# Performance work log

Hardware: AMD Instinct MI355X
Metric: run time of the kernel (lower is better)

## Reference

```python
import jax, jax.numpy as jnp
import numpy as np

N1 = 8192; N2 = 8192; E = 131072
D_IN = 128; H = 256; T = 32; B = 16
GCN_DIMS = [(D_IN, H), (H, H), (H, H)]


def _gcn_conv(x, edge_index, W):
    # PyG GCNConv (bias=False): add self-loops, symmetric D^-1/2 (A+I) D^-1/2 normalization.
    n = x.shape[0]
    h = x @ W
    loop = jnp.arange(n, dtype=edge_index.dtype)
    src = jnp.concatenate([edge_index[0], loop])
    dst = jnp.concatenate([edge_index[1], loop])
    deg = jax.ops.segment_sum(jnp.ones(dst.shape[0], h.dtype), dst, num_segments=n)
    dinv = jnp.where(deg > 0, jax.lax.rsqrt(deg), 0.0)
    norm = dinv[src] * dinv[dst]
    return jax.ops.segment_sum(norm[:, None] * h[src], dst, num_segments=n)


def _layer(f1, f2, ei1, ei2, Wg, Wu, bu, last):
    c1 = _gcn_conv(f1, ei1, Wg)
    c2 = _gcn_conv(f2, ei2, Wg)
    sim = f1 @ f2.T                      # [N1, N2] 'dot' similarity
    a1 = jax.nn.softmax(sim, axis=1)     # row softmax
    a2 = jax.nn.softmax(sim, axis=0)     # col softmax
    att1 = a1 @ f2                       # [N1, d]
    att2 = a2.T @ f1                     # [N2, d]
    g1 = jnp.concatenate([c1, f1, f1 - att1], axis=1) @ Wu + bu
    g2 = jnp.concatenate([c2, f2, f2 - att2], axis=1) @ Wu + bu
    if last:
        return g1, g2                    # last layer: no tanh, no dropout
    return jnp.tanh(g1), jnp.tanh(g2)    # dropout is a no-op in eval mode


def _forward(f1, f2, ei1, ei2, avg_v, gcn_Ws, upd_Ws, upd_bs,
             gated_W, gated_b, tn_W, tn_Wb, tn_b, fc1_W, fc1_b, sc_W, sc_b):
    n_layers = len(gcn_Ws)
    for i in range(n_layers):
        f1, f2 = _layer(f1, f2, ei1, ei2, gcn_Ws[i], upd_Ws[i], upd_bs[i],
                        last=(i == n_layers - 1))
    # gated readout: sum(sigmoid(gated(x)) * x)
    p1 = jnp.sum(jax.nn.sigmoid(f1 @ gated_W + gated_b) * f1, axis=0)  # [H]
    p2 = jnp.sum(jax.nn.sigmoid(f2 @ gated_W + gated_b) * f2, axis=0)  # [H]
    # NTN (TensorNetworkModule)
    scoring = jnp.einsum('i,ijt,j->t', p1, tn_W, p2)                   # bilinear term [T]
    block = tn_Wb @ jnp.concatenate([p1, p2])                          # [T]
    ntn = jax.nn.relu(scoring + block + tn_b)
    s = jnp.tanh(ntn @ fc1_W + fc1_b)                                  # [B]
    score = jax.nn.sigmoid(s @ sc_W + sc_b)                            # [1]
    pre_ged = -jnp.log(score) * avg_v                                  # target_mode='exp'
    return score.reshape(-1), pre_ged.reshape(-1)


def setup_inputs():
    key = jax.random.key(0)
    ks = jax.random.split(key, 32)
    rn = lambda k, sh, s=0.05: jax.random.normal(k, sh, dtype=jnp.float32) * s
    inp = {
        'features_1': jax.random.normal(ks[0], (N1, D_IN), dtype=jnp.float32),
        'features_2': jax.random.normal(ks[1], (N2, D_IN), dtype=jnp.float32),
        'edge_index_1': jax.random.randint(ks[2], (2, E), 0, N1, dtype=jnp.int32),
        'edge_index_2': jax.random.randint(ks[3], (2, E), 0, N2, dtype=jnp.int32),
        'avg_v': jnp.full((1,), 12.0, dtype=jnp.float32),
    }
    for i, (di, do) in enumerate(GCN_DIMS):
        inp[f'gcn_W{i}'] = rn(ks[4 + i], (di, do))
        inp[f'upd_W{i}'] = rn(ks[8 + i], (2 * di + do, do))
        inp[f'upd_b{i}'] = jnp.zeros((do,), jnp.float32)
    inp['gated_W'] = rn(ks[12], (H, H)); inp['gated_b'] = jnp.zeros((H,), jnp.float32)
    inp['tn_W'] = rn(ks[13], (H, H, T))
    inp['tn_Wb'] = rn(ks[14], (T, 2 * H)); inp['tn_b'] = jnp.zeros((T,), jnp.float32)
    inp['fc1_W'] = rn(ks[15], (T, B)); inp['fc1_b'] = jnp.zeros((B,), jnp.float32)
    inp['sc_W'] = rn(ks[16], (B, 1)); inp['sc_b'] = jnp.zeros((1,), jnp.float32)
    return inp


def reference(features_1, features_2, edge_index_1, edge_index_2, avg_v,
              gcn_W0, gcn_W1, gcn_W2, upd_W0, upd_W1, upd_W2,
              upd_b0, upd_b1, upd_b2, gated_W, gated_b,
              tn_W, tn_Wb, tn_b, fc1_W, fc1_b, sc_W, sc_b):
    return _forward(features_1, features_2, edge_index_1, edge_index_2, avg_v,
                    [gcn_W0, gcn_W1, gcn_W2], [upd_W0, upd_W1, upd_W2],
                    [upd_b0, upd_b1, upd_b2], gated_W, gated_b,
                    tn_W, tn_Wb, tn_b, fc1_W, fc1_b, sc_W, sc_b)
```

## Files before the change

kernel.cpp:

```cpp
#include <hip/hip_runtime.h>
#include <hip/hip_bf16.h>
#include <stdint.h>

#define NN 8192
#define EDG 131072
#define NSPLIT 4

typedef __attribute__((ext_vector_type(8))) short bf16x8;
typedef __attribute__((ext_vector_type(4))) float f32x4;
typedef unsigned short us;

__device__ __forceinline__ us f2bf(float f) {
  union { float f; unsigned u; } v; v.f = f;
  return (us)((v.u + 0x7fffu + ((v.u >> 16) & 1u)) >> 16);
}

__device__ __forceinline__ us f2bf_trunc(float f) {
  union { float f; unsigned u; } v; v.f = f;
  return (us)(v.u >> 16);
}

__device__ __forceinline__ float bf2f(us u) {
  union { unsigned u; float f; } v; v.u = ((unsigned)u) << 16;
  return v.f;
}

__device__ __forceinline__ void load_lds16(const void* g, void* l) {
  __builtin_amdgcn_global_load_lds(
      (__attribute__((address_space(1))) void*)(uintptr_t)g,
      (__attribute__((address_space(3))) void*)(uintptr_t)l,
      16, 0, 0);
}

template <int EPI>
__global__ __launch_bounds__(256) void gemm_k(
    const us* __restrict__ A, int lda, const us* __restrict__ Bt, int ldb,
    const float* __restrict__ bias, void* __restrict__ Cv, int ldc, int K) {
  __shared__ alignas(16) us As[64 * 32];
  __shared__ alignas(16) us Bs[128 * 32];
  const int t = threadIdx.x;
  const int wave = t >> 6, lane = t & 63;
  const int wrow = wave * 16;
  const int lrow = lane & 15, quad = lane >> 4;
  const int rowBase = blockIdx.x * 64;
  const int colBase = blockIdx.y * 128;
  const int sr = t >> 2, sch = t & 3;

  f32x4 acc[8];
#pragma unroll
  for (int j = 0; j < 8; j++) acc[j] = f32x4{0.f, 0.f, 0.f, 0.f};

  for (int kb = 0; kb < K; kb += 32) {
    __syncthreads();
    const us* asrc = A + (size_t)(rowBase + sr) * lda + kb + sch * 8;
    load_lds16(asrc, (char*)As + t * 16);
    const us* bsrc = Bt + (size_t)(colBase + sr) * ldb + kb + sch * 8;
    load_lds16(bsrc, (char*)Bs + t * 16);
    load_lds16(bsrc + (size_t)64 * ldb, (char*)Bs + t * 16 + 4096);
    __syncthreads();
    bf16x8 af = *(const bf16x8*)&As[(wrow + lrow) * 32 + quad * 8];
#pragma unroll
    for (int j = 0; j < 8; j++) {
      bf16x8 bfr = *(const bf16x8*)&Bs[(j * 16 + lrow) * 32 + quad * 8];
      acc[j] = __builtin_amdgcn_mfma_f32_16x16x32_bf16(af, bfr, acc[j], 0, 0, 0);
    }
  }

#pragma unroll
  for (int j = 0; j < 8; j++) {
    int col = colBase + j * 16 + lrow;
#pragma unroll
    for (int r = 0; r < 4; r++) {
      int row = rowBase + wrow + quad * 4 + r;
      size_t idx = (size_t)row * ldc + col;
      float v = acc[j][r];
      if (EPI == 0) ((float*)Cv)[idx] = v;
      else if (EPI == 2) ((float*)Cv)[idx] = v + bias[col];
      else if (EPI == 4) ((us*)Cv)[idx] = f2bf(v + bias[col]);
      else ((us*)Cv)[idx] = f2bf(tanhf(v + bias[col]));
    }
  }
}

template <int DIN>
__global__ __launch_bounds__(256, (DIN == 128) ? 3 : 2) void flash_att(
    const us* __restrict__ Q, const us* __restrict__ K,
    const us* __restrict__ Vt, us* __restrict__ Opart,
    float* __restrict__ mpart, float* __restrict__ lpart, int kvPerSplit) {
  constexpr int NKC = DIN / 32;
  constexpr int OJ = DIN / 16;
  __shared__ alignas(16) us As[2][64 * 32];
  __shared__ alignas(16) us KB[2][128 * 32];
  __shared__ alignas(16) us Vs[2][DIN * 32];
  us* Ps = &KB[0][0];

  const int t = threadIdx.x;
  const int wave = t >> 6, lane = t & 63;
  const int wrow = wave * 16;
  const int lrow = lane & 15, quad = lane >> 4;
  const int rowBase = blockIdx.x * 64;
  const int split = blockIdx.y;
  const int kv0 = split * kvPerSplit;
  const int sr = t >> 2, sch = t & 3;
  const int pkey = ((lrow >> 2) ^ lrow) & 3;

  auto stageQ = [&](int kc, int buf) {
    const us* qsrc = Q + (size_t)(rowBase + sr) * DIN + kc * 32 + sch * 8;
    load_lds16(qsrc, (char*)&As[buf][0] + t * 16);
  };
  auto stageK = [&](int kt, int kc, int buf) {
    const us* ksrc = K + (size_t)(kt + sr) * DIN + kc * 32 + sch * 8;
    load_lds16(ksrc, (char*)&KB[buf][0] + t * 16);
    load_lds16(ksrc + (size_t)64 * DIN, (char*)&KB[buf][0] + t * 16 + 4096);
  };
  auto stageV = [&](int kt, int cc, int buf) {
#pragma unroll
    for (int p = 0; p < DIN / 64; p++) {
      const us* vsrc = Vt + (size_t)(p * 64 + sr) * NN + kt + cc * 32 + sch * 8;
      load_lds16(vsrc, (char*)&Vs[buf][0] + p * 4096 + t * 16);
    }
  };

  stageQ(0, 0);
  stageV(kv0, 0, 0);

  float m_i[4], l_i[4];
#pragma unroll
  for (int r = 0; r < 4; r++) { m_i[r] = -3.0e38f; l_i[r] = 0.f; }
  f32x4 accO[OJ];
#pragma unroll
  for (int j = 0; j < OJ; j++) accO[j] = f32x4{0.f, 0.f, 0.f, 0.f};

  for (int kt = kv0; kt < kv0 + kvPerSplit; kt += 128) {
    __syncthreads();
    stageK(kt, 0, 0);

    f32x4 accS[8];
#pragma unroll
    for (int j = 0; j < 8; j++) accS[j] = f32x4{0.f, 0.f, 0.f, 0.f};
    for (int kc = 0; kc < NKC; kc++) {
      const int buf = kc & 1;
      __syncthreads();
      if (kc + 1 < NKC) { stageK(kt, kc + 1, buf ^ 1); stageQ(kc + 1, buf ^ 1); }
      bf16x8 af = *(const bf16x8*)&As[buf][(wrow + lrow) * 32 + quad * 8];
#pragma unroll
      for (int j = 0; j < 8; j++) {
        bf16x8 bfr = *(const bf16x8*)&KB[buf][(j * 16 + lrow) * 32 + quad * 8];
        accS[j] = __builtin_amdgcn_mfma_f32_16x16x32_bf16(af, bfr, accS[j], 0, 0, 0);
      }
    }

    float alpha[4];
#pragma unroll
    for (int r = 0; r < 4; r++) {
      float v = accS[0][r];
#pragma unroll
      for (int j = 1; j < 8; j++) v = fmaxf(v, accS[j][r]);
#pragma unroll
      for (int mask = 1; mask < 16; mask <<= 1) v = fmaxf(v, __shfl_xor(v, mask));
      float mn = fmaxf(m_i[r], v);
      alpha[r] = __expf(m_i[r] - mn);
      m_i[r] = mn;
    }
    __syncthreads();
    float ts[4] = {0.f, 0.f, 0.f, 0.f};
#pragma unroll
    for (int j = 0; j < 8; j++)
#pragma unroll
      for (int r = 0; r < 4; r++) {
        float p = __expf(accS[j][r] - m_i[r]);
        ts[r] += p;
        int prow = wrow + quad * 4 + r;
        int key = (quad ^ r) & 3;
        int g = (j * 16 + lrow) >> 3;
        Ps[prow * 128 + ((g ^ (key << 1)) << 3) + (lrow & 7)] = f2bf_trunc(p);
      }
#pragma unroll
    for (int r = 0; r < 4; r++) {
      float v = ts[r];
#pragma unroll
      for (int mask = 1; mask < 16; mask <<= 1) v += __shfl_xor(v, mask);
      l_i[r] = l_i[r] * alpha[r] + v;
    }
#pragma unroll
    for (int j = 0; j < OJ; j++)
#pragma unroll
      for (int r = 0; r < 4; r++) accO[j][r] *= alpha[r];

    const bool hasNext = (kt + 128 < kv0 + kvPerSplit);
    for (int cc = 0; cc < 4; cc++) {
      if (cc) __syncthreads();
      if (cc + 1 < 4) stageV(kt, cc + 1, (cc + 1) & 1);
      else if (hasNext) { stageV(kt + 128, 0, 0); stageQ(0, 0); }
      const int gk = cc * 4 + quad;
      bf16x8 af = *(const bf16x8*)&Ps[(wrow + lrow) * 128 + ((gk ^ (pkey << 1)) << 3)];
      const us* vb = &Vs[cc & 1][0];
#pragma unroll
      for (int j = 0; j < OJ; j++) {
        bf16x8 bfr = *(const bf16x8*)&vb[(j * 16 + lrow) * 32 + quad * 8];
        accO[j] = __builtin_amdgcn_mfma_f32_16x16x32_bf16(af, bfr, accO[j], 0, 0, 0);
      }
    }
  }

#pragma unroll
  for (int j = 0; j < OJ; j++)
#pragma unroll
    for (int r = 0; r < 4; r++) {
      int row = rowBase + wrow + quad * 4 + r;
      int col = j * 16 + lrow;
      Opart[((size_t)split * NN + row) * DIN + col] = f2bf(accO[j][r]);
    }
  if (lrow == 0) {
#pragma unroll
    for (int r = 0; r < 4; r++) {
      int row = rowBase + wrow + quad * 4 + r;
      mpart[(size_t)split * NN + row] = m_i[r];
      lpart[(size_t)split * NN + row] = l_i[r];
    }
  }
}

__global__ void merge_cat(const us* __restrict__ Op, const float* __restrict__ mp,
                          const float* __restrict__ lp, const float* __restrict__ cbuf,
                          const us* __restrict__ fbf, us* __restrict__ cat,
                          int din, int W) {
  int i = blockIdx.y;
  int c = blockIdx.x * 256 + threadIdx.x;
  us o;
  if (c < 256) {
    o = f2bf(cbuf[(size_t)i * 256 + c]);
  } else if (c < 256 + din) {
    o = fbf[(size_t)i * din + (c - 256)];
  } else {
    int f = c - 256 - din;
    float m[NSPLIT], w[NSPLIT];
    float M = -3.0e38f;
#pragma unroll
    for (int s = 0; s < NSPLIT; s++) { m[s] = mp[(size_t)s * NN + i]; M = fmaxf(M, m[s]); }
    float L = 0.f;
#pragma unroll
    for (int s = 0; s < NSPLIT; s++) { w[s] = __expf(m[s] - M); L += lp[(size_t)s * NN + i] * w[s]; }
    float a = 0.f;
#pragma unroll
    for (int s = 0; s < NSPLIT; s++)
      a += w[s] * bf2f(Op[((size_t)s * NN + i) * din + f]);
    o = f2bf(bf2f(fbf[(size_t)i * din + f]) - a / L);
  }
  cat[(size_t)i * W + c] = o;
}


__global__ void ws_sentinel(float* out) { out[0] = 12345.0f; out[1] = 12345.0f; }

__global__ void cvt_bf16(const float* __restrict__ in, us* __restrict__ out, int n) {
  int i = (blockIdx.x * 256 + threadIdx.x) * 4;
  if (i < n) {
    f32x4 v = *(const f32x4*)(in + i);
    uint2 p;
    p.x = f2bf(v.x) | ((unsigned)f2bf(v.y) << 16);
    p.y = f2bf(v.z) | ((unsigned)f2bf(v.w) << 16);
    *(uint2*)(out + i) = p;
  }
}

__global__ void transpose_bf16(const float* __restrict__ src, us* __restrict__ dst,
                               int R, int C) {
  __shared__ float tile[32][33];
  int c0 = blockIdx.x * 32, r0 = blockIdx.y * 32;
  int x = threadIdx.x, y = threadIdx.y;
  for (int i = y; i < 32; i += 8) tile[i][x] = src[(size_t)(r0 + i) * C + c0 + x];
  __syncthreads();
  for (int i = y; i < 32; i += 8) dst[(size_t)(c0 + i) * R + r0 + x] = f2bf(tile[x][i]);
}

__global__ void transpose_bb(const us* __restrict__ src, us* __restrict__ dst,
                             int R, int C) {
  __shared__ us tile[32][33];
  int c0 = blockIdx.x * 32, r0 = blockIdx.y * 32;
  int x = threadIdx.x, y = threadIdx.y;
  for (int i = y; i < 32; i += 8) tile[i][x] = src[(size_t)(r0 + i) * C + c0 + x];
  __syncthreads();
  for (int i = y; i < 32; i += 8) dst[(size_t)(c0 + i) * R + r0 + x] = tile[x][i];
}

__global__ void deg_count(const int* __restrict__ dst, int* __restrict__ deg) {
  int e = blockIdx.x * 256 + threadIdx.x;
  atomicAdd(&deg[dst[e]], 1);
}

__global__ void make_dinv(const int* __restrict__ deg, float* __restrict__ dinv) {
  int v = blockIdx.x * 256 + threadIdx.x;
  dinv[v] = rsqrtf((float)(deg[v] + 1));
}

__global__ void scan_deg(const int* __restrict__ deg, int* __restrict__ rowstart) {
  __shared__ int part[1024];
  int t = threadIdx.x;
  int base = t * 8;
  int local[8];
  int s = 0;
#pragma unroll
  for (int i = 0; i < 8; i++) { local[i] = s; s += deg[base + i]; }
  part[t] = s;
  __syncthreads();
  for (int off = 1; off < 1024; off <<= 1) {
    int v = (t >= off) ? part[t - off] : 0;
    __syncthreads();
    part[t] += v;
    __syncthreads();
  }
  int offset = (t == 0) ? 0 : part[t - 1];
#pragma unroll
  for (int i = 0; i < 8; i++) rowstart[base + i] = offset + local[i];
  if (t == 1023) rowstart[8192] = offset + s;
}

__global__ void csr_fill(const int* __restrict__ src, const int* __restrict__ dst,
                         int* __restrict__ cursor, int* __restrict__ csr_src) {
  int e = blockIdx.x * 256 + threadIdx.x;
  int pos = atomicAdd(&cursor[dst[e]], 1);
  csr_src[pos] = src[e];
}

__global__ __launch_bounds__(256) void gcn_agg(
    const int* __restrict__ rowstart, const int* __restrict__ csr_src,
    const float* __restrict__ dinv, const float* __restrict__ h,
    float* __restrict__ c) {
  int node = blockIdx.x * 4 + (threadIdx.x >> 6);
  int lane = threadIdx.x & 63;
  float dn = dinv[node];
  f32x4 acc = *(const f32x4*)(h + (size_t)node * 256 + lane * 4);
  float w0 = dn * dn;
  acc.x *= w0; acc.y *= w0; acc.z *= w0; acc.w *= w0;
  int s0 = rowstart[node], s1 = rowstart[node + 1];
  for (int j = s0; j < s1; j++) {
    int s = csr_src[j];
    float w = dinv[s] * dn;
    f32x4 v = *(const f32x4*)(h + (size_t)s * 256 + lane * 4);
    acc.x += w * v.x; acc.y += w * v.y; acc.z += w * v.z; acc.w += w * v.w;
  }
  *(f32x4*)(c + (size_t)node * 256 + lane * 4) = acc;
}

__global__ void gated_pool(const float* __restrict__ q, const us* __restrict__ f,
                           float* __restrict__ p) {
  int col = threadIdx.x;
  int r0 = blockIdx.x * 128;
  float a = 0.f;
  for (int i = r0; i < r0 + 128; i++) {
    float qv = q[(size_t)i * 256 + col];
    a += bf2f(f[(size_t)i * 256 + col]) / (1.f + __expf(-qv));
  }
  atomicAdd(&p[col], a);
}

__global__ void ntn_bilinear(const float* __restrict__ p1, const float* __restrict__ tnW,
                             float* __restrict__ tmp) {
  int c = blockIdx.x * 256 + threadIdx.x;
  float a = 0.f;
#pragma unroll 8
  for (int i = 0; i < 256; i++) a += p1[i] * tnW[(size_t)i * 8192 + c];
  tmp[c] = a;
}

__global__ void ntn_final(const float* __restrict__ tmp, const float* __restrict__ p1,
                          const float* __restrict__ p2, const float* __restrict__ tnWb,
                          const float* __restrict__ tnb, const float* __restrict__ fc1W,
                          const float* __restrict__ fc1b, const float* __restrict__ scW,
                          const float* __restrict__ scb, const float* __restrict__ avgv,
                          float* __restrict__ out) {
  __shared__ float pc[512];
  __shared__ float ntn[32];
  __shared__ float sarr[16];
  int t = threadIdx.x;
  pc[t] = p1[t];
  pc[256 + t] = p2[t];
  __syncthreads();
  if (t < 32) {
    float sc = 0.f;
    for (int j = 0; j < 256; j++) sc += tmp[j * 32 + t] * pc[256 + j];
    float bl = 0.f;
    for (int k = 0; k < 512; k++) bl += tnWb[t * 512 + k] * pc[k];
    float v = sc + bl + tnb[t];
    ntn[t] = v > 0.f ? v : 0.f;
  }
  __syncthreads();
  if (t < 16) {
    float a = fc1b[t];
    for (int i = 0; i < 32; i++) a += ntn[i] * fc1W[i * 16 + t];
    sarr[t] = tanhf(a);
  }
  __syncthreads();
  if (t == 0) {
    float a = scb[0];
    for (int b = 0; b < 16; b++) a += sarr[b] * scW[b];
    float score = 1.f / (1.f + expf(-a));
    out[0] = score;
    out[1] = -logf(score) * avgv[0];
  }
}


extern "C" void kernel_launch(void* const* d_in, const int* in_sizes, int n_in,
                              void* d_out, int out_size, void* d_ws, size_t ws_size,
                              hipStream_t stream) {
  (void)in_sizes; (void)n_in; (void)out_size;
  const float* feat1 = (const float*)d_in[0];
  const float* feat2 = (const float*)d_in[1];
  const int* ei1 = (const int*)d_in[2];
  const int* ei2 = (const int*)d_in[3];
  const float* avgv = (const float*)d_in[4];
  const float* gcnW[3] = {(const float*)d_in[5], (const float*)d_in[8], (const float*)d_in[11]};
  const float* updW[3] = {(const float*)d_in[6], (const float*)d_in[9], (const float*)d_in[12]};
  const float* updb[3] = {(const float*)d_in[7], (const float*)d_in[10], (const float*)d_in[13]};
  const float* gatedW = (const float*)d_in[14];
  const float* gatedb = (const float*)d_in[15];
  const float* tnW = (const float*)d_in[16];
  const float* tnWb = (const float*)d_in[17];
  const float* tnb = (const float*)d_in[18];
  const float* fc1W = (const float*)d_in[19];
  const float* fc1b = (const float*)d_in[20];
  const float* scW = (const float*)d_in[21];
  const float* scb = (const float*)d_in[22];
  float* out = (float*)d_out;

  char* wp = (char*)d_ws;
  auto take = [&](size_t b) { char* p = wp; wp += (b + 255) & ~(size_t)255; return p; };
  us* Op = (us*)take((size_t)NSPLIT * NN * 256 * 2);
  us* cat1 = (us*)take((size_t)NN * 768 * 2);
  us* cat2 = (us*)take((size_t)NN * 768 * 2);
  us* fA1 = (us*)take((size_t)NN * 256 * 2);
  us* fA2 = (us*)take((size_t)NN * 256 * 2);
  us* fB1 = (us*)take((size_t)NN * 256 * 2);
  us* fB2 = (us*)take((size_t)NN * 256 * 2);
  us* f1bT = (us*)take((size_t)NN * 256 * 2);
  us* f2bT = (us*)take((size_t)NN * 256 * 2);
  float* h1 = (float*)take((size_t)NN * 256 * 4);
  float* h2 = (float*)take((size_t)NN * 256 * 4);
  float* c1 = (float*)take((size_t)NN * 256 * 4);
  float* c2 = (float*)take((size_t)NN * 256 * 4);
  us* WgT[3], *WuT[3];
  for (int l = 0; l < 3; l++) WgT[l] = (us*)take(256 * 256 * 2);
  for (int l = 0; l < 3; l++) WuT[l] = (us*)take(256 * 768 * 2);
  us* gWT = (us*)take(256 * 256 * 2);
  int* deg1 = (int*)take(NN * 4);
  int* deg2 = (int*)take(NN * 4);
  float* dinv1 = (float*)take(NN * 4);
  float* dinv2 = (float*)take(NN * 4);
  int* rs1 = (int*)take((NN + 1) * 4);
  int* rs2 = (int*)take((NN + 1) * 4);
  int* cur1 = (int*)take(NN * 4);
  int* cur2 = (int*)take(NN * 4);
  int* csr1 = (int*)take((size_t)EDG * 4);
  int* csr2 = (int*)take((size_t)EDG * 4);
  float* mp = (float*)take((size_t)NSPLIT * NN * 4);
  float* lp = (float*)take((size_t)NSPLIT * NN * 4);
  float* p1 = (float*)take(1024);
  float* p2 = (float*)take(1024);
  float* tmp = (float*)take(NN * 4);

  size_t need = (size_t)(wp - (char*)d_ws);
  if (need > ws_size) {
    ws_sentinel<<<1, 1, 0, stream>>>(out);
    return;
  }

  hipMemsetAsync(deg1, 0, NN * 4, stream);
  hipMemsetAsync(deg2, 0, NN * 4, stream);
  deg_count<<<EDG / 256, 256, 0, stream>>>(ei1 + EDG, deg1);
  deg_count<<<EDG / 256, 256, 0, stream>>>(ei2 + EDG, deg2);
  make_dinv<<<NN / 256, 256, 0, stream>>>(deg1, dinv1);
  make_dinv<<<NN / 256, 256, 0, stream>>>(deg2, dinv2);
  scan_deg<<<1, 1024, 0, stream>>>(deg1, rs1);
  scan_deg<<<1, 1024, 0, stream>>>(deg2, rs2);
  hipMemcpyAsync(cur1, rs1, NN * 4, hipMemcpyDeviceToDevice, stream);
  hipMemcpyAsync(cur2, rs2, NN * 4, hipMemcpyDeviceToDevice, stream);
  csr_fill<<<EDG / 256, 256, 0, stream>>>(ei1, ei1 + EDG, cur1, csr1);
  csr_fill<<<EDG / 256, 256, 0, stream>>>(ei2, ei2 + EDG, cur2, csr2);

  for (int l = 0; l < 3; l++) {
    int din = (l == 0) ? 128 : 256;
    int W = 256 + 2 * din;
    transpose_bf16<<<dim3(8, din / 32), dim3(32, 8), 0, stream>>>(gcnW[l], WgT[l], din, 256);
    transpose_bf16<<<dim3(8, W / 32), dim3(32, 8), 0, stream>>>(updW[l], WuT[l], W, 256);
  }
  transpose_bf16<<<dim3(8, 8), dim3(32, 8), 0, stream>>>(gatedW, gWT, 256, 256);

  us* f1 = fA1; us* f2 = fA2;
  us* fn1 = fB1; us* fn2 = fB2;
  cvt_bf16<<<NN * 128 / 1024, 256, 0, stream>>>(feat1, f1, NN * 128);
  cvt_bf16<<<NN * 128 / 1024, 256, 0, stream>>>(feat2, f2, NN * 128);

  for (int l = 0; l < 3; l++) {
    const int din = (l == 0) ? 128 : 256;
    const int W = 256 + 2 * din;

    if (l == 0) {
      transpose_bf16<<<dim3(din / 32, NN / 32), dim3(32, 8), 0, stream>>>(feat1, f1bT, NN, din);
      transpose_bf16<<<dim3(din / 32, NN / 32), dim3(32, 8), 0, stream>>>(feat2, f2bT, NN, din);
    } else {
      transpose_bb<<<dim3(din / 32, NN / 32), dim3(32, 8), 0, stream>>>(f1, f1bT, NN, din);
      transpose_bb<<<dim3(din / 32, NN / 32), dim3(32, 8), 0, stream>>>(f2, f2bT, NN, din);
    }

    gemm_k<0><<<dim3(128, 2), 256, 0, stream>>>(f1, din, WgT[l], din, nullptr, h1, 256, din);
    gemm_k<0><<<dim3(128, 2), 256, 0, stream>>>(f2, din, WgT[l], din, nullptr, h2, 256, din);

    gcn_agg<<<NN / 4, 256, 0, stream>>>(rs1, csr1, dinv1, h1, c1);
    gcn_agg<<<NN / 4, 256, 0, stream>>>(rs2, csr2, dinv2, h2, c2);

    if (l == 0) {
      flash_att<128><<<dim3(NN / 64, NSPLIT), 256, 0, stream>>>(f1, f2, f2bT, Op, mp, lp, NN / NSPLIT);
      merge_cat<<<dim3(W / 256, NN), 256, 0, stream>>>(Op, mp, lp, c1, f1, cat1, din, W);
      flash_att<128><<<dim3(NN / 64, NSPLIT), 256, 0, stream>>>(f2, f1, f1bT, Op, mp, lp, NN / NSPLIT);
      merge_cat<<<dim3(W / 256, NN), 256, 0, stream>>>(Op, mp, lp, c2, f2, cat2, din, W);
    } else {
      flash_att<256><<<dim3(NN / 64, NSPLIT), 256, 0, stream>>>(f1, f2, f2bT, Op, mp, lp, NN / NSPLIT);
      merge_cat<<<dim3(W / 256, NN), 256, 0, stream>>>(Op, mp, lp, c1, f1, cat1, din, W);
      flash_att<256><<<dim3(NN / 64, NSPLIT), 256, 0, stream>>>(f2, f1, f1bT, Op, mp, lp, NN / NSPLIT);
      merge_cat<<<dim3(W / 256, NN), 256, 0, stream>>>(Op, mp, lp, c2, f2, cat2, din, W);
    }

    if (l < 2) {
      gemm_k<5><<<dim3(128, 2), 256, 0, stream>>>(cat1, W, WuT[l], W, updb[l], fn1, 256, W);
      gemm_k<5><<<dim3(128, 2), 256, 0, stream>>>(cat2, W, WuT[l], W, updb[l], fn2, 256, W);
    } else {
      gemm_k<4><<<dim3(128, 2), 256, 0, stream>>>(cat1, W, WuT[l], W, updb[l], fn1, 256, W);
      gemm_k<4><<<dim3(128, 2), 256, 0, stream>>>(cat2, W, WuT[l], W, updb[l], fn2, 256, W);
    }
    us* s;
    s = f1; f1 = fn1; fn1 = s;
    s = f2; f2 = fn2; fn2 = s;
  }

  gemm_k<2><<<dim3(128, 2), 256, 0, stream>>>(f1, 256, gWT, 256, gatedb, c1, 256, 256);
  gemm_k<2><<<dim3(128, 2), 256, 0, stream>>>(f2, 256, gWT, 256, gatedb, c2, 256, 256);
  hipMemsetAsync(p1, 0, 256 * 4, stream);
  hipMemsetAsync(p2, 0, 256 * 4, stream);
  gated_pool<<<64, 256, 0, stream>>>(c1, f1, p1);
  gated_pool<<<64, 256, 0, stream>>>(c2, f2, p2);

  ntn_bilinear<<<32, 256, 0, stream>>>(p1, tnW, tmp);
  ntn_final<<<1, 256, 0, stream>>>(tmp, p1, p2, tnWb, tnb, fc1W, fc1b, scW, scb, avgv, out);
}
```

Measured before the change: 1.209 ms.

## Batch both graphs into single launches and store GCN intermediates in bf16

Each pair of per-graph kernels (gemm, transpose, gcn aggregation, flash attention, merge, pooling, CSR build) becomes one launch, with a grid dimension selecting graph 1 or 2. This removes launch overhead and doubles the grid size, which helps fill the GPU on small kernels. The GCN path now keeps h and the aggregated output in bf16 and folds the source-side dinv scaling into the gemm epilogue. That halves gather traffic but adds bf16 rounding on the intermediates. The attention Op/m/l buffers are doubled so both directions can run concurrently.

```diff
diff --git a/kernel.cpp b/kernel.cpp
--- a/kernel.cpp
+++ b/kernel.cpp
@@ -33,11 +33,16 @@
 }
 
 template <int EPI>
-__global__ __launch_bounds__(256) void gemm_k(
-    const us* __restrict__ A, int lda, const us* __restrict__ Bt, int ldb,
-    const float* __restrict__ bias, void* __restrict__ Cv, int ldc, int K) {
+__global__ __launch_bounds__(256) void gemm2(
+    const us* __restrict__ A1, const us* __restrict__ A2, int lda,
+    const us* __restrict__ Bt, int ldb,
+    const float* __restrict__ b1, const float* __restrict__ b2,
+    void* __restrict__ C1, void* __restrict__ C2, int ldc, int K) {
   __shared__ alignas(16) us As[64 * 32];
   __shared__ alignas(16) us Bs[128 * 32];
+  const us* A = blockIdx.z ? A2 : A1;
+  const float* bias = blockIdx.z ? b2 : b1;
+  void* Cv = blockIdx.z ? C2 : C1;
   const int t = threadIdx.x;
   const int wave = t >> 6, lane = t & 63;
   const int wrow = wave * 16;
@@ -77,22 +82,32 @@
       if (EPI == 0) ((float*)Cv)[idx] = v;
       else if (EPI == 2) ((float*)Cv)[idx] = v + bias[col];
       else if (EPI == 4) ((us*)Cv)[idx] = f2bf(v + bias[col]);
-      else ((us*)Cv)[idx] = f2bf(tanhf(v + bias[col]));
+      else if (EPI == 5) ((us*)Cv)[idx] = f2bf(tanhf(v + bias[col]));
+      else ((us*)Cv)[idx] = f2bf(v * bias[row]);
     }
   }
 }
 
 template <int DIN>
 __global__ __launch_bounds__(256, (DIN == 128) ? 3 : 2) void flash_att(
-    const us* __restrict__ Q, const us* __restrict__ K,
-    const us* __restrict__ Vt, us* __restrict__ Opart,
-    float* __restrict__ mpart, float* __restrict__ lpart, int kvPerSplit) {
+    const us* __restrict__ f1, const us* __restrict__ f2,
+    const us* __restrict__ f1T, const us* __restrict__ f2T,
+    us* __restrict__ Op, float* __restrict__ mp, float* __restrict__ lp,
+    int kvPerSplit) {
   constexpr int NKC = DIN / 32;
   constexpr int OJ = DIN / 16;
   __shared__ alignas(16) us As[2][64 * 32];
   __shared__ alignas(16) us KB[2][128 * 32];
   __shared__ alignas(16) us Vs[2][DIN * 32];
   us* Ps = &KB[0][0];
+
+  const int dir = blockIdx.z;
+  const us* Q = dir ? f2 : f1;
+  const us* K = dir ? f1 : f2;
+  const us* Vt = dir ? f1T : f2T;
+  us* Opart = Op + (size_t)dir * NSPLIT * NN * DIN;
+  float* mpart = mp + (size_t)dir * NSPLIT * NN;
+  float* lpart = lp + (size_t)dir * NSPLIT * NN;
 
   const int t = threadIdx.x;
   const int wave = t >> 6, lane = t & 63;
@@ -172,7 +187,7 @@
         ts[r] += p;
         int prow = wrow + quad * 4 + r;
         int key = (quad ^ r) & 3;
-        int g = (j * 16 + lrow) >> 3;
+        int g = 2 * j + (lrow >> 3);
         Ps[prow * 128 + ((g ^ (key << 1)) << 3) + (lrow & 7)] = f2bf_trunc(p);
       }
 #pragma unroll
@@ -222,14 +237,23 @@
 }
 
 __global__ void merge_cat(const us* __restrict__ Op, const float* __restrict__ mp,
-                          const float* __restrict__ lp, const float* __restrict__ cbuf,
-                          const us* __restrict__ fbf, us* __restrict__ cat,
+                          const float* __restrict__ lp,
+                          const us* __restrict__ cb1, const us* __restrict__ cb2,
+                          const us* __restrict__ f1, const us* __restrict__ f2,
+                          us* __restrict__ cat1, us* __restrict__ cat2,
                           int din, int W) {
+  const int z = blockIdx.z;
+  const us* Ops = Op + (size_t)z * NSPLIT * NN * din;
+  const float* mm = mp + (size_t)z * NSPLIT * NN;
+  const float* ll = lp + (size_t)z * NSPLIT * NN;
+  const us* cbuf = z ? cb2 : cb1;
+  const us* fbf = z ? f2 : f1;
+  us* cat = z ? cat2 : cat1;
   int i = blockIdx.y;
   int c = blockIdx.x * 256 + threadIdx.x;
   us o;
   if (c < 256) {
-    o = f2bf(cbuf[(size_t)i * 256 + c]);
+    o = cbuf[(size_t)i * 256 + c];
   } else if (c < 256 + din) {
     o = fbf[(size_t)i * din + (c - 256)];
   } else {
@@ -237,14 +261,14 @@
     float m[NSPLIT], w[NSPLIT];
     float M = -3.0e38f;
 #pragma unroll
-    for (int s = 0; s < NSPLIT; s++) { m[s] = mp[(size_t)s * NN + i]; M = fmaxf(M, m[s]); }
+    for (int s = 0; s < NSPLIT; s++) { m[s] = mm[(size_t)s * NN + i]; M = fmaxf(M, m[s]); }
     float L = 0.f;
 #pragma unroll
-    for (int s = 0; s < NSPLIT; s++) { w[s] = __expf(m[s] - M); L += lp[(size_t)s * NN + i] * w[s]; }
+    for (int s = 0; s < NSPLIT; s++) { w[s] = __expf(m[s] - M); L += ll[(size_t)s * NN + i] * w[s]; }
     float a = 0.f;
 #pragma unroll
     for (int s = 0; s < NSPLIT; s++)
-      a += w[s] * bf2f(Op[((size_t)s * NN + i) * din + f]);
+      a += w[s] * bf2f(Ops[((size_t)s * NN + i) * din + f]);
     o = f2bf(bf2f(fbf[(size_t)i * din + f]) - a / L);
   }
   cat[(size_t)i * W + c] = o;
@@ -253,7 +277,10 @@
 
 __global__ void ws_sentinel(float* out) { out[0] = 12345.0f; out[1] = 12345.0f; }
 
-__global__ void cvt_bf16(const float* __restrict__ in, us* __restrict__ out, int n) {
+__global__ void cvt2(const float* __restrict__ i1, const float* __restrict__ i2,
+                     us* __restrict__ o1, us* __restrict__ o2, int n) {
+  const float* in = blockIdx.y ? i2 : i1;
+  us* out = blockIdx.y ? o2 : o1;
   int i = (blockIdx.x * 256 + threadIdx.x) * 4;
   if (i < n) {
     f32x4 v = *(const f32x4*)(in + i);
@@ -274,27 +301,50 @@
   for (int i = y; i < 32; i += 8) dst[(size_t)(c0 + i) * R + r0 + x] = f2bf(tile[x][i]);
 }
 
-__global__ void transpose_bb(const us* __restrict__ src, us* __restrict__ dst,
-                             int R, int C) {
-  __shared__ us tile[32][33];
+__global__ void transpose_bf2(const float* __restrict__ s1, const float* __restrict__ s2,
+                              us* __restrict__ d1, us* __restrict__ d2, int R, int C) {
+  __shared__ float tile[32][33];
+  const float* src = blockIdx.z ? s2 : s1;
+  us* dst = blockIdx.z ? d2 : d1;
   int c0 = blockIdx.x * 32, r0 = blockIdx.y * 32;
   int x = threadIdx.x, y = threadIdx.y;
   for (int i = y; i < 32; i += 8) tile[i][x] = src[(size_t)(r0 + i) * C + c0 + x];
   __syncthreads();
+  for (int i = y; i < 32; i += 8) dst[(size_t)(c0 + i) * R + r0 + x] = f2bf(tile[x][i]);
+}
+
+__global__ void transpose_bb2(const us* __restrict__ s1, const us* __restrict__ s2,
+                              us* __restrict__ d1, us* __restrict__ d2, int R, int C) {
+  __shared__ us tile[32][33];
+  const us* src = blockIdx.z ? s2 : s1;
+  us* dst = blockIdx.z ? d2 : d1;
+  int c0 = blockIdx.x * 32, r0 = blockIdx.y * 32;
+  int x = threadIdx.x, y = threadIdx.y;
+  for (int i = y; i < 32; i += 8) tile[i][x] = src[(size_t)(r0 + i) * C + c0 + x];
+  __syncthreads();
   for (int i = y; i < 32; i += 8) dst[(size_t)(c0 + i) * R + r0 + x] = tile[x][i];
 }
 
-__global__ void deg_count(const int* __restrict__ dst, int* __restrict__ deg) {
+__global__ void deg_count2(const int* __restrict__ d1, const int* __restrict__ d2,
+                           int* __restrict__ g1, int* __restrict__ g2) {
+  const int* dst = blockIdx.y ? d2 : d1;
+  int* deg = blockIdx.y ? g2 : g1;
   int e = blockIdx.x * 256 + threadIdx.x;
   atomicAdd(&deg[dst[e]], 1);
 }
 
-__global__ void make_dinv(const int* __restrict__ deg, float* __restrict__ dinv) {
+__global__ void make_dinv2(const int* __restrict__ g1, const int* __restrict__ g2,
+                           float* __restrict__ o1, float* __restrict__ o2) {
+  const int* deg = blockIdx.y ? g2 : g1;
+  float* dinv = blockIdx.y ? o2 : o1;
   int v = blockIdx.x * 256 + threadIdx.x;
   dinv[v] = rsqrtf((float)(deg[v] + 1));
 }
 
-__global__ void scan_deg(const int* __restrict__ deg, int* __restrict__ rowstart) {
+__global__ void scan_deg2(const int* __restrict__ g1, const int* __restrict__ g2,
+                          int* __restrict__ r1, int* __restrict__ r2) {
+  const int* deg = blockIdx.x ? g2 : g1;
+  int* rowstart = blockIdx.x ? r2 : r1;
   __shared__ int part[1024];
   int t = threadIdx.x;
   int base = t * 8;
@@ -316,35 +366,54 @@
   if (t == 1023) rowstart[8192] = offset + s;
 }
 
-__global__ void csr_fill(const int* __restrict__ src, const int* __restrict__ dst,
-                         int* __restrict__ cursor, int* __restrict__ csr_src) {
+__global__ void csr_fill2(const int* __restrict__ e1, const int* __restrict__ e2,
+                          int* __restrict__ cu1, int* __restrict__ cu2,
+                          int* __restrict__ c1, int* __restrict__ c2) {
+  const int* ei = blockIdx.y ? e2 : e1;
+  int* cursor = blockIdx.y ? cu2 : cu1;
+  int* csr_src = blockIdx.y ? c2 : c1;
   int e = blockIdx.x * 256 + threadIdx.x;
-  int pos = atomicAdd(&cursor[dst[e]], 1);
-  csr_src[pos] = src[e];
-}
-
-__global__ __launch_bounds__(256) void gcn_agg(
-    const int* __restrict__ rowstart, const int* __restrict__ csr_src,
-    const float* __restrict__ dinv, const float* __restrict__ h,
-    float* __restrict__ c) {
+  int pos = atomicAdd(&cursor[ei[EDG + e]], 1);
+  csr_src[pos] = ei[e];
+}
+
+__global__ __launch_bounds__(256) void gcn_agg2(
+    const int* __restrict__ r1, const int* __restrict__ r2,
+    const int* __restrict__ cs1, const int* __restrict__ cs2,
+    const float* __restrict__ d1, const float* __restrict__ d2,
+    const us* __restrict__ h1, const us* __restrict__ h2,
+    us* __restrict__ o1, us* __restrict__ o2) {
+  const int* rowstart = blockIdx.y ? r2 : r1;
+  const int* csr_src = blockIdx.y ? cs2 : cs1;
+  const float* dinv = blockIdx.y ? d2 : d1;
+  const us* hs = blockIdx.y ? h2 : h1;
+  us* c = blockIdx.y ? o2 : o1;
   int node = blockIdx.x * 4 + (threadIdx.x >> 6);
   int lane = threadIdx.x & 63;
-  float dn = dinv[node];
-  f32x4 acc = *(const f32x4*)(h + (size_t)node * 256 + lane * 4);
-  float w0 = dn * dn;
-  acc.x *= w0; acc.y *= w0; acc.z *= w0; acc.w *= w0;
+  const us* hp = hs + lane * 4;
+  uint2 u = *(const uint2*)(hp + (size_t)node * 256);
+  float a0 = bf2f(u.x & 0xffffu), a1 = bf2f(u.x >> 16);
+  float a2 = bf2f(u.y & 0xffffu), a3 = bf2f(u.y >> 16);
   int s0 = rowstart[node], s1 = rowstart[node + 1];
   for (int j = s0; j < s1; j++) {
     int s = csr_src[j];
-    float w = dinv[s] * dn;
-    f32x4 v = *(const f32x4*)(h + (size_t)s * 256 + lane * 4);
-    acc.x += w * v.x; acc.y += w * v.y; acc.z += w * v.z; acc.w += w * v.w;
-  }
-  *(f32x4*)(c + (size_t)node * 256 + lane * 4) = acc;
-}
-
-__global__ void gated_pool(const float* __restrict__ q, const us* __restrict__ f,
-                           float* __restrict__ p) {
+    uint2 v = *(const uint2*)(hp + (size_t)s * 256);
+    a0 += bf2f(v.x & 0xffffu); a1 += bf2f(v.x >> 16);
+    a2 += bf2f(v.y & 0xffffu); a3 += bf2f(v.y >> 16);
+  }
+  float dn = dinv[node];
+  uint2 o;
+  o.x = f2bf(a0 * dn) | ((unsigned)f2bf(a1 * dn) << 16);
+  o.y = f2bf(a2 * dn) | ((unsigned)f2bf(a3 * dn) << 16);
+  *(uint2*)(c + (size_t)node * 256 + lane * 4) = o;
+}
+
+__global__ void gated_pool2(const float* __restrict__ q1, const float* __restrict__ q2,
+                            const us* __restrict__ f1, const us* __restrict__ f2,
+                            float* __restrict__ o1, float* __restrict__ o2) {
+  const float* q = blockIdx.y ? q2 : q1;
+  const us* f = blockIdx.y ? f2 : f1;
+  float* p = blockIdx.y ? o2 : o1;
   int col = threadIdx.x;
   int r0 = blockIdx.x * 128;
   float a = 0.f;
@@ -427,19 +496,21 @@
 
   char* wp = (char*)d_ws;
   auto take = [&](size_t b) { char* p = wp; wp += (b + 255) & ~(size_t)255; return p; };
-  us* Op = (us*)take((size_t)NSPLIT * NN * 256 * 2);
+  us* Op = (us*)take((size_t)2 * NSPLIT * NN * 256 * 2);
   us* cat1 = (us*)take((size_t)NN * 768 * 2);
   us* cat2 = (us*)take((size_t)NN * 768 * 2);
+  float* q1 = (float*)cat1;
+  float* q2 = (float*)cat2;
   us* fA1 = (us*)take((size_t)NN * 256 * 2);
   us* fA2 = (us*)take((size_t)NN * 256 * 2);
   us* fB1 = (us*)take((size_t)NN * 256 * 2);
   us* fB2 = (us*)take((size_t)NN * 256 * 2);
   us* f1bT = (us*)take((size_t)NN * 256 * 2);
   us* f2bT = (us*)take((size_t)NN * 256 * 2);
-  float* h1 = (float*)take((size_t)NN * 256 * 4);
-  float* h2 = (float*)take((size_t)NN * 256 * 4);
-  float* c1 = (float*)take((size_t)NN * 256 * 4);
-  float* c2 = (float*)take((size_t)NN * 256 * 4);
+  us* hs1 = (us*)take((size_t)NN * 256 * 2);
+  us* hs2 = (us*)take((size_t)NN * 256 * 2);
+  us* cb1 = (us*)take((size_t)NN * 256 * 2);
+  us* cb2 = (us*)take((size_t)NN * 256 * 2);
   us* WgT[3], *WuT[3];
   for (int l = 0; l < 3; l++) WgT[l] = (us*)take(256 * 256 * 2);
   for (int l = 0; l < 3; l++) WuT[l] = (us*)take(256 * 768 * 2);
@@ -454,8 +525,8 @@
   int* cur2 = (int*)take(NN * 4);
   int* csr1 = (int*)take((size_t)EDG * 4);
   int* csr2 = (int*)take((size_t)EDG * 4);
-  float* mp = (float*)take((size_t)NSPLIT * NN * 4);
-  float* lp = (float*)take((size_t)NSPLIT * NN * 4);
+  float* mp = (float*)take((size_t)2 * NSPLIT * NN * 4);
+  float* lp = (float*)take((size_t)2 * NSPLIT * NN * 4);
   float* p1 = (float*)take(1024);
   float* p2 = (float*)take(1024);
   float* tmp = (float*)take(NN * 4);
@@ -468,16 +539,12 @@
 
   hipMemsetAsync(deg1, 0, NN * 4, stream);
   hipMemsetAsync(deg2, 0, NN * 4, stream);
-  deg_count<<<EDG / 256, 256, 0, stream>>>(ei1 + EDG, deg1);
-  deg_count<<<EDG / 256, 256, 0, stream>>>(ei2 + EDG, deg2);
-  make_dinv<<<NN / 256, 256, 0, stream>>>(deg1, dinv1);
-  make_dinv<<<NN / 256, 256, 0, stream>>>(deg2, dinv2);
-  scan_deg<<<1, 1024, 0, stream>>>(deg1, rs1);
-  scan_deg<<<1, 1024, 0, stream>>>(deg2, rs2);
+  deg_count2<<<dim3(EDG / 256, 2), 256, 0, stream>>>(ei1 + EDG, ei2 + EDG, deg1, deg2);
+  make_dinv2<<<dim3(NN / 256, 2), 256, 0, stream>>>(deg1, deg2, dinv1, dinv2);
+  scan_deg2<<<2, 1024, 0, stream>>>(deg1, deg2, rs1, rs2);
   hipMemcpyAsync(cur1, rs1, NN * 4, hipMemcpyDeviceToDevice, stream);
   hipMemcpyAsync(cur2, rs2, NN * 4, hipMemcpyDeviceToDevice, stream);
-  csr_fill<<<EDG / 256, 256, 0, stream>>>(ei1, ei1 + EDG, cur1, csr1);
-  csr_fill<<<EDG / 256, 256, 0, stream>>>(ei2, ei2 + EDG, cur2, csr2);
+  csr_fill2<<<dim3(EDG / 256, 2), 256, 0, stream>>>(ei1, ei2, cur1, cur2, csr1, csr2);
 
   for (int l = 0; l < 3; l++) {
     int din = (l == 0) ? 128 : 256;
@@ -489,57 +556,40 @@
 
   us* f1 = fA1; us* f2 = fA2;
   us* fn1 = fB1; us* fn2 = fB2;
-  cvt_bf16<<<NN * 128 / 1024, 256, 0, stream>>>(feat1, f1, NN * 128);
-  cvt_bf16<<<NN * 128 / 1024, 256, 0, stream>>>(feat2, f2, NN * 128);
+  cvt2<<<dim3(NN * 128 / 1024, 2), 256, 0, stream>>>(feat1, feat2, f1, f2, NN * 128);
 
   for (int l = 0; l < 3; l++) {
     const int din = (l == 0) ? 128 : 256;
     const int W = 256 + 2 * din;
 
-    if (l == 0) {
-      transpose_bf16<<<dim3(din / 32, NN / 32), dim3(32, 8), 0, stream>>>(feat1, f1bT, NN, din);
-      transpose_bf16<<<dim3(din / 32, NN / 32), dim3(32, 8), 0, stream>>>(feat2, f2bT, NN, din);
-    } else {
-      transpose_bb<<<dim3(din / 32, NN / 32), dim3(32, 8), 0, stream>>>(f1, f1bT, NN, din);
-      transpose_bb<<<dim3(din / 32, NN / 32), dim3(32, 8), 0, stream>>>(f2, f2bT, NN, din);
-    }
-
-    gemm_k<0><<<dim3(128, 2), 256, 0, stream>>>(f1, din, WgT[l], din, nullptr, h1, 256, din);
-    gemm_k<0><<<dim3(128, 2), 256, 0, stream>>>(f2, din, WgT[l], din, nullptr, h2, 256, din);
-
-    gcn_agg<<<NN / 4, 256, 0, stream>>>(rs1, csr1, dinv1, h1, c1);
-    gcn_agg<<<NN / 4, 256, 0, stream>>>(rs2, csr2, dinv2, h2, c2);
-
-    if (l == 0) {
-      flash_att<128><<<dim3(NN / 64, NSPLIT), 256, 0, stream>>>(f1, f2, f2bT, Op, mp, lp, NN / NSPLIT);
-      merge_cat<<<dim3(W / 256, NN), 256, 0, stream>>>(Op, mp, lp, c1, f1, cat1, din, W);
-      flash_att<128><<<dim3(NN / 64, NSPLIT), 256, 0, stream>>>(f2, f1, f1bT, Op, mp, lp, NN / NSPLIT);
-      merge_cat<<<dim3(W / 256, NN), 256, 0, stream>>>(Op, mp, lp, c2, f2, cat2, din, W);
-    } else {
-      flash_att<256><<<dim3(NN / 64, NSPLIT), 256, 0, stream>>>(f1, f2, f2bT, Op, mp, lp, NN / NSPLIT);
-      merge_cat<<<dim3(W / 256, NN), 256, 0, stream>>>(Op, mp, lp, c1, f1, cat1, din, W);
-      flash_att<256><<<dim3(NN / 64, NSPLIT), 256, 0, stream>>>(f2, f1, f1bT, Op, mp, lp, NN / NSPLIT);
-      merge_cat<<<dim3(W / 256, NN), 256, 0, stream>>>(Op, mp, lp, c2, f2, cat2, din, W);
-    }
-
-    if (l < 2) {
-      gemm_k<5><<<dim3(128, 2), 256, 0, stream>>>(cat1, W, WuT[l], W, updb[l], fn1, 256, W);
-      gemm_k<5><<<dim3(128, 2), 256, 0, stream>>>(cat2, W, WuT[l], W, updb[l], fn2, 256, W);
-    } else {
-      gemm_k<4><<<dim3(128, 2), 256, 0, stream>>>(cat1, W, WuT[l], W, updb[l], fn1, 256, W);
-      gemm_k<4><<<dim3(128, 2), 256, 0, stream>>>(cat2, W, WuT[l], W, updb[l], fn2, 256, W);
-    }
+    if (l == 0)
+      transpose_bf2<<<dim3(din / 32, NN / 32, 2), dim3(32, 8), 0, stream>>>(feat1, feat2, f1bT, f2bT, NN, din);
+    else
+      transpose_bb2<<<dim3(din / 32, NN / 32, 2), dim3(32, 8), 0, stream>>>(f1, f2, f1bT, f2bT, NN, din);
+
+    gemm2<6><<<dim3(128, 2, 2), 256, 0, stream>>>(f1, f2, din, WgT[l], din, dinv1, dinv2, hs1, hs2, 256, din);
+
+    gcn_agg2<<<dim3(NN / 4, 2), 256, 0, stream>>>(rs1, rs2, csr1, csr2, dinv1, dinv2, hs1, hs2, cb1, cb2);
+
+    if (l == 0)
+      flash_att<128><<<dim3(NN / 64, NSPLIT, 2), 256, 0, stream>>>(f1, f2, f1bT, f2bT, Op, mp, lp, NN / NSPLIT);
+    else
+      flash_att<256><<<dim3(NN / 64, NSPLIT, 2), 256, 0, stream>>>(f1, f2, f1bT, f2bT, Op, mp, lp, NN / NSPLIT);
+    merge_cat<<<dim3(W / 256, NN, 2), 256, 0, stream>>>(Op, mp, lp, cb1, cb2, f1, f2, cat1, cat2, din, W);
+
+    if (l < 2)
+      gemm2<5><<<dim3(128, 2, 2), 256, 0, stream>>>(cat1, cat2, W, WuT[l], W, updb[l], updb[l], fn1, fn2, 256, W);
+    else
+      gemm2<4><<<dim3(128, 2, 2), 256, 0, stream>>>(cat1, cat2, W, WuT[l], W, updb[l], updb[l], fn1, fn2, 256, W);
     us* s;
     s = f1; f1 = fn1; fn1 = s;
     s = f2; f2 = fn2; fn2 = s;
   }
 
-  gemm_k<2><<<dim3(128, 2), 256, 0, stream>>>(f1, 256, gWT, 256, gatedb, c1, 256, 256);
-  gemm_k<2><<<dim3(128, 2), 256, 0, stream>>>(f2, 256, gWT, 256, gatedb, c2, 256, 256);
+  gemm2<2><<<dim3(128, 2, 2), 256, 0, stream>>>(f1, f2, 256, gWT, 256, gatedb, gatedb, q1, q2, 256, 256);
   hipMemsetAsync(p1, 0, 256 * 4, stream);
   hipMemsetAsync(p2, 0, 256 * 4, stream);
-  gated_pool<<<64, 256, 0, stream>>>(c1, f1, p1);
-  gated_pool<<<64, 256, 0, stream>>>(c2, f2, p2);
+  gated_pool2<<<dim3(64, 2), 256, 0, stream>>>(q1, q2, f1, f2, p1, p2);
 
   ntn_bilinear<<<32, 256, 0, stream>>>(p1, tnW, tmp);
   ntn_final<<<1, 256, 0, stream>>>(tmp, p1, p2, tnWb, tnb, fc1W, fc1b, scW, scb, avgv, out);
```

After: 1.073 ms. 11.2% less time.
